# Kernel tuning notes

Measured on AMD Instinct MI355X. Metric: run time of the kernel, lower is better.

## Reference

```python
import jax, jax.numpy as jnp
import numpy as np
from jax import lax

B = 8192          # batched independent VAD frames (original module is batch=1 streaming)
CUTOFF = 129      # STFT_CUTOFF
STRIDE = 128      # STFT_STRIDE
NFFT = 256        # STFT kernel length (inferred: pad 576->640, stride 128 -> 4 frames)
H = 128           # LSTM hidden size


def conv1d(x, w, b=None, stride=1, padding=0):
    # x: [B, Cin, T], w: [Cout, Cin, K]
    y = lax.conv_general_dilated(x, w, (stride,), [(padding, padding)],
                                 dimension_numbers=("NCH", "OIH", "NCH"))
    if b is not None:
        y = y + b[None, :, None]
    return y


def setup_inputs() -> dict:
    key = jax.random.key(0)
    ks = jax.random.split(key, 40)
    f32 = jnp.float32

    def rn(i, shape, scale=0.1):
        return jax.random.normal(ks[i], shape, dtype=f32) * scale

    inp = {
        "audio": jax.random.normal(ks[0], (B, 576), dtype=f32),
        "h": jnp.zeros((B, H), dtype=f32),
        "c": jnp.zeros((B, H), dtype=f32),
        # STFT basis: 129 real + 129 imag cosine/sine rows, kernel 256
        "forward_basis": rn(1, (2 * CUTOFF, 1, NFFT), 0.1),
        # encoder: 4 conv1d+relu blocks (Silero v5 layout)
        "enc_w1": rn(2, (128, 129, 3)), "enc_b1": rn(3, (128,)),
        "enc_w2": rn(4, (64, 128, 3)), "enc_b2": rn(5, (64,)),
        "enc_w3": rn(6, (64, 64, 3)),  "enc_b3": rn(7, (64,)),
        "enc_w4": rn(8, (128, 64, 3)), "enc_b4": rn(9, (128,)),
        # LSTM cell weights
        "wi": rn(10, (H, H)), "wf": rn(11, (H, H)), "wg": rn(12, (H, H)), "wo": rn(13, (H, H)),
        "ui": rn(14, (H, H)), "uf": rn(15, (H, H)), "ug": rn(16, (H, H)), "uo": rn(17, (H, H)),
        "bxi": rn(18, (H,)), "bxf": rn(19, (H,)), "bxg": rn(20, (H,)), "bxo": rn(21, (H,)),
        "bhi": rn(22, (H,)), "bhf": rn(23, (H,)), "bhg": rn(24, (H,)), "bho": rn(25, (H,)),
        # output head: conv1d 128 -> 1, kernel 1
        "conv_w": rn(26, (1, H, 1)), "conv_b": rn(27, (1,)),
    }
    return inp


def reference(audio, h, c, forward_basis,
              enc_w1, enc_b1, enc_w2, enc_b2, enc_w3, enc_b3, enc_w4, enc_b4,
              wi, wf, wg, wo, ui, uf, ug, uo,
              bxi, bxf, bxg, bxo, bhi, bhf, bhg, bho,
              conv_w, conv_b):
    # STFT via strided conv1d on reflect-padded audio
    x = jnp.pad(audio, ((0, 0), (0, 64)), mode="reflect")[:, None, :]   # [B,1,640]
    x = conv1d(x, forward_basis, stride=STRIDE)                          # [B,258,4]
    real, imag = x[:, :CUTOFF, :], x[:, CUTOFF:, :]
    mag = jnp.sqrt(real ** 2 + imag ** 2)                                # [B,129,4]

    # encoder: conv+relu stack, T: 4 -> 4 -> 2 -> 1 -> 1
    e = jax.nn.relu(conv1d(mag, enc_w1, enc_b1, stride=1, padding=1))
    e = jax.nn.relu(conv1d(e, enc_w2, enc_b2, stride=2, padding=1))
    e = jax.nn.relu(conv1d(e, enc_w3, enc_b3, stride=2, padding=1))
    e = jax.nn.relu(conv1d(e, enc_w4, enc_b4, stride=1, padding=1))
    x = e[:, :, 0]                                                       # [B,128]

    lin = lambda v, W, b: v @ W.T + b
    i_gate = jax.nn.sigmoid(lin(x, wi, bxi) + lin(h, ui, bhi))
    f_gate = jax.nn.sigmoid(lin(x, wf, bxf) + lin(h, uf, bhf))
    g_gate = jnp.tanh(lin(x, wg, bxg) + lin(h, ug, bhg))
    o_gate = jax.nn.sigmoid(lin(x, wo, bxo) + lin(h, uo, bho))
    c_out = f_gate * c + i_gate * g_gate
    h_out = o_gate * jnp.tanh(c_out)

    # output head: relu -> conv1d(128->1, k=1) -> sigmoid -> mean over T(=1)
    y = jax.nn.relu(h_out)                                               # [B,128]
    logit = y @ conv_w[0, :, 0] + conv_b[0]                              # [B]
    prob = jax.nn.sigmoid(logit)[:, None]                                # [B,1]
    return prob, h_out, c_out
```

## Files before the change

### kernel.cpp

```cpp
#include <hip/hip_runtime.h>
#include <math.h>

#define BATCH 8192
typedef unsigned short u16;
typedef unsigned int u32;
typedef __attribute__((ext_vector_type(8))) short bf16x8;
typedef __attribute__((ext_vector_type(4))) float f32x4;
typedef __attribute__((ext_vector_type(4))) unsigned short u16x4;

__device__ __forceinline__ float sigm(float v) { return 1.0f / (1.0f + __expf(-v)); }
__device__ __forceinline__ u16 f2bf(float f) {
    union { float f; u32 u; } v; v.f = f;
    u32 r = v.u + 0x7FFFu + ((v.u >> 16) & 1u);
    return (u16)(r >> 16);
}
__device__ __forceinline__ float bf2f(u16 h) {
    union { u32 u; float f; } v; v.u = ((u32)h) << 16; return v.f;
}
__device__ __forceinline__ void split_store4(float4 v, u16* hp, u16* lp) {
    u16 h0 = f2bf(v.x), h1 = f2bf(v.y), h2 = f2bf(v.z), h3 = f2bf(v.w);
    u16x4 hv = {h0, h1, h2, h3};
    u16x4 lv = {f2bf(v.x - bf2f(h0)), f2bf(v.y - bf2f(h1)),
                f2bf(v.z - bf2f(h2)), f2bf(v.w - bf2f(h3))};
    *(u16x4*)hp = hv; *(u16x4*)lp = lv;
}
__device__ __forceinline__ bf16x8 bfrag(const u16* Bf, int nt, int ch, int nch, int lane) {
    return *(const bf16x8*)(Bf + (((size_t)nt * nch + ch) * 64 + lane) * 8);
}
#define MFMA(a, b, c) __builtin_amdgcn_mfma_f32_16x16x32_bf16(a, b, c, 0, 0, 0)

#define S_FBT 69632
#define S_B1  61440
#define S_B2A 16384
#define S_B2B 24576
#define S_B3  8192
#define S_B4  8192
#define S_BL  131072
#define P_FBT 0
#define P_B1  139264
#define P_B2A 262144
#define P_B2B 294912
#define P_B3  344064
#define P_B4  360448
#define P_BL  376832
#define N_PREP 319488

__global__ __launch_bounds__(256) void k_prep(const float* __restrict__ fb,
                                              const float* __restrict__ w1, const float* __restrict__ w2,
                                              const float* __restrict__ w3, const float* __restrict__ w4,
                                              const float* __restrict__ wi, const float* __restrict__ wf,
                                              const float* __restrict__ wg, const float* __restrict__ wo,
                                              const float* __restrict__ ui, const float* __restrict__ uf,
                                              const float* __restrict__ ug, const float* __restrict__ uo,
                                              u16* __restrict__ wsu) {
    const float* Ws[8] = {wi, wf, wg, wo, ui, uf, ug, uo};
    for (int i = blockIdx.x * 256 + threadIdx.x; i < N_PREP; i += gridDim.x * 256) {
        int r = i;
        float v; int P, S, idx;
        if (r < S_FBT) {
            int f = r >> 9, lane = (r & 511) >> 3, e = r & 7;
            int n = (f >> 3) * 16 + (lane & 15), k = (f & 7) * 32 + (lane >> 4) * 8 + e;
            int c = n >> 1, part = n & 1;
            v = (n < 258) ? fb[(size_t)(c + part * 129) * 256 + k] : 0.f;
            P = P_FBT; S = S_FBT; idx = r;
        } else if ((r -= S_FBT) < S_B1) {
            int kk = r / 20480, r2 = r - kk * 20480;
            int f = r2 >> 9, lane = (r2 & 511) >> 3, e = r2 & 7;
            int n = (f / 5) * 16 + (lane & 15), k = (f % 5) * 32 + (lane >> 4) * 8 + e;
            v = (k < 129) ? w1[(size_t)n * 387 + k * 3 + kk] : 0.f;
            P = P_B1; S = S_B1; idx = r;
        } else if ((r -= S_B1) < S_B2A) {
            int f = r >> 9, lane = (r & 511) >> 3, e = r & 7;
            int n = (f >> 3) * 16 + (lane & 15), k = (f & 7) * 32 + (lane >> 4) * 8 + e;
            v = w2[(size_t)n * 384 + (k & 127) * 3 + (k >> 7) + 1];
            P = P_B2A; S = S_B2A; idx = r;
        } else if ((r -= S_B2A) < S_B2B) {
            int f = r >> 9, lane = (r & 511) >> 3, e = r & 7;
            int n = (f / 12) * 16 + (lane & 15), k = (f % 12) * 32 + (lane >> 4) * 8 + e;
            v = w2[(size_t)n * 384 + (k & 127) * 3 + (k >> 7)];
            P = P_B2B; S = S_B2B; idx = r;
        } else if ((r -= S_B2B) < S_B3) {
            int f = r >> 9, lane = (r & 511) >> 3, e = r & 7;
            int n = (f >> 2) * 16 + (lane & 15), k = (f & 3) * 32 + (lane >> 4) * 8 + e;
            v = w3[(size_t)n * 192 + (k & 63) * 3 + (k >> 6) + 1];
            P = P_B3; S = S_B3; idx = r;
        } else if ((r -= S_B3) < S_B4) {
            int f = r >> 9, lane = (r & 511) >> 3, e = r & 7;
            int n = (f >> 1) * 16 + (lane & 15), k = (f & 1) * 32 + (lane >> 4) * 8 + e;
            v = w4[(size_t)n * 192 + k * 3 + 1];
            P = P_B4; S = S_B4; idx = r;
        } else {
            r -= S_B4;
            int f = r >> 9, lane = (r & 511) >> 3, e = r & 7;
            int n = (f >> 3) * 16 + (lane & 15), k = (f & 7) * 32 + (lane >> 4) * 8 + e;
            int g = n >> 7, j = n & 127;
            v = Ws[g + ((k >= 128) ? 4 : 0)][(size_t)j * 128 + (k & 127)];
            P = P_BL; S = S_BL; idx = r;
        }
        u16 h = f2bf(v);
        wsu[P + idx] = h;
        wsu[P + S + idx] = f2bf(v - bf2f(h));
    }
}

__global__ __launch_bounds__(512) void k_all(const float* __restrict__ audio,
                                             const u16* __restrict__ wsu,
                                             const float* __restrict__ hin, const float* __restrict__ cin,
                                             const float* __restrict__ b1, const float* __restrict__ b2,
                                             const float* __restrict__ b3, const float* __restrict__ b4,
                                             const float* __restrict__ bxi, const float* __restrict__ bxf,
                                             const float* __restrict__ bxg, const float* __restrict__ bxo,
                                             const float* __restrict__ bhi, const float* __restrict__ bhf,
                                             const float* __restrict__ bhg, const float* __restrict__ bho,
                                             const float* __restrict__ cw, const float* __restrict__ cb,
                                             float* __restrict__ out) {
    __shared__ __align__(16) u16 uni[32256];
    u16* aAh = uni;
    u16* aAl = uni + 11520;
    u16* mAh = uni;
    u16* mAl = uni + 16128;
    u16* eAh = uni;
    u16* eAl = uni + 8320;
    u16* s2h = uni + 16640;
    u16* s2l = uni + 18816;
    u16* s3h = uni + 20992;
    u16* s3l = uni + 22144;
    u16* xhh = uni + 23296;
    u16* xhl = uni + 27520;
    float* pr = (float*)(uni + 31744);
    const int tid = threadIdx.x;
    const int b0 = blockIdx.x << 4;
    for (int i = tid; i < 16 * 160; i += 512) {
        int bb = i / 160, j4 = (i - bb * 160) * 4;
        const float* ap = audio + (size_t)(b0 + bb) * 576;
        float4 v;
        if (j4 < 576) v = *(const float4*)(ap + j4);
        else { v.x = ap[1150 - j4]; v.y = ap[1149 - j4]; v.z = ap[1148 - j4]; v.w = ap[1147 - j4]; }
        int phys = bb * 720 + j4 + (j4 >> 7) * 8;
        split_store4(v, aAh + phys, aAl + phys);
    }
    __syncthreads();
    const int lane = tid & 63, w = tid >> 6;
    const int m = lane & 15, quad = lane >> 4;
    const u16* fbT = wsu + P_FBT;
    const int tcnt = (w == 7) ? 3 : 2;
    f32x4 acc[4][3];
    #pragma unroll
    for (int mt = 0; mt < 4; ++mt)
        #pragma unroll
        for (int t = 0; t < 3; ++t) acc[mt][t] = (f32x4){0.f, 0.f, 0.f, 0.f};
    for (int ch = 0; ch < 8; ++ch) {
        bf16x8 ah[4], al[4];
        #pragma unroll
        for (int mt = 0; mt < 4; ++mt) {
            int Rm = mt * 16 + m;
            int phys = (Rm >> 2) * 720 + (Rm & 3) * 136 + ch * 32 + quad * 8 + ((ch >= 4) ? 8 : 0);
            ah[mt] = *(const bf16x8*)(aAh + phys);
            al[mt] = *(const bf16x8*)(aAl + phys);
        }
        #pragma unroll
        for (int tt = 0; tt < 3; ++tt) {
            if (tt < tcnt) {
                int t = w * 2 + tt;
                bf16x8 bh = bfrag(fbT, t, ch, 8, lane);
                bf16x8 bl_ = bfrag(fbT + S_FBT, t, ch, 8, lane);
                #pragma unroll
                for (int mt = 0; mt < 4; ++mt) {
                    acc[mt][tt] = MFMA(ah[mt], bh, acc[mt][tt]);
                    acc[mt][tt] = MFMA(ah[mt], bl_, acc[mt][tt]);
                    acc[mt][tt] = MFMA(al[mt], bh, acc[mt][tt]);
                }
            }
        }
    }
    __syncthreads();
    for (int i = tid; i < 16128; i += 512) ((u32*)uni)[i] = 0u;
    __syncthreads();
    #pragma unroll
    for (int tt = 0; tt < 3; ++tt) {
        if (tt < tcnt) {
            int n = (w * 2 + tt) * 16 + m;
            #pragma unroll
            for (int mt = 0; mt < 4; ++mt)
                #pragma unroll
                for (int r = 0; r < 4; ++r) {
                    float vv = acc[mt][tt][r];
                    float s = vv * vv;
                    s += __shfl_xor(s, 1);
                    if (!(n & 1)) {
                        int R = mt * 16 + quad * 4 + r;
                        int bb = R >> 2, t = R & 3, c = n >> 1;
                        float sv = sqrtf(s);
                        u16 h = f2bf(sv);
                        int phys = (bb * 6 + t + 1) * 168 + c;
                        mAh[phys] = h;
                        mAl[phys] = f2bf(sv - bf2f(h));
                    }
                }
        }
    }
    __syncthreads();
    const u16* B1h = wsu + P_B1;
    const u16* B1l = wsu + P_B1 + S_B1;
    f32x4 acc2[4];
    #pragma unroll
    for (int mt = 0; mt < 4; ++mt) acc2[mt] = (f32x4){0.f, 0.f, 0.f, 0.f};
    for (int kk = 0; kk < 3; ++kk) {
        for (int ch = 0; ch < 5; ++ch) {
            bf16x8 bh = bfrag(B1h + kk * 20480, w, ch, 5, lane);
            bf16x8 bl_ = bfrag(B1l + kk * 20480, w, ch, 5, lane);
            #pragma unroll
            for (int mt = 0; mt < 4; ++mt) {
                int Rm = mt * 16 + m;
                int phys = ((Rm >> 2) * 6 + (Rm & 3) + kk) * 168 + ch * 32 + quad * 8;
                bf16x8 ah = *(const bf16x8*)(mAh + phys);
                bf16x8 al = *(const bf16x8*)(mAl + phys);
                acc2[mt] = MFMA(ah, bh, acc2[mt]);
                acc2[mt] = MFMA(ah, bl_, acc2[mt]);
                acc2[mt] = MFMA(al, bh, acc2[mt]);
            }
        }
    }
    __syncthreads();
    {
        int n = w * 16 + m;
        float bv = b1[n];
        #pragma unroll
        for (int mt = 0; mt < 4; ++mt)
            #pragma unroll
            for (int r = 0; r < 4; ++r) {
                int R = mt * 16 + quad * 4 + r;
                float vv = fmaxf(acc2[mt][r] + bv, 0.f);
                u16 h = f2bf(vv);
                int phys = (R >> 2) * 520 + (R & 3) * 128 + n;
                eAh[phys] = h;
                eAl[phys] = f2bf(vv - bf2f(h));
            }
    }
    for (int i = tid; i < 16 * 32; i += 512) {
        int row = i >> 5, c4 = (i & 31) * 4;
        float4 v = *(const float4*)(hin + (size_t)(b0 + row) * 128 + c4);
        split_store4(v, xhh + row * 264 + 128 + c4, xhl + row * 264 + 128 + c4);
    }
    __syncthreads();
    {
        const int isB = w >> 2, nt = w & 3;
        const int awoff = isB ? 128 : 0;
        const int nch = isB ? 12 : 8;
        const u16* Bh = wsu + (isB ? P_B2B : P_B2A);
        const u16* Bl = Bh + (isB ? S_B2B : S_B2A);
        f32x4 a2 = (f32x4){0.f, 0.f, 0.f, 0.f};
        for (int ch = 0; ch < nch; ++ch) {
            int phys = m * 520 + awoff + ch * 32 + quad * 8;
            bf16x8 ah = *(const bf16x8*)(eAh + phys);
            bf16x8 al = *(const bf16x8*)(eAl + phys);
            bf16x8 bh = bfrag(Bh, nt, ch, nch, lane);
            bf16x8 bl_ = bfrag(Bl, nt, ch, nch, lane);
            a2 = MFMA(ah, bh, a2);
            a2 = MFMA(ah, bl_, a2);
            a2 = MFMA(al, bh, a2);
        }
        const int oc = nt * 16 + m;
        const float bv = b2[oc];
        const int col = isB * 64 + oc;
        #pragma unroll
        for (int r = 0; r < 4; ++r) {
            int row = quad * 4 + r;
            float vv = fmaxf(a2[r] + bv, 0.f);
            u16 h = f2bf(vv);
            s2h[row * 136 + col] = h;
            s2l[row * 136 + col] = f2bf(vv - bf2f(h));
        }
    }
    __syncthreads();
    if (w < 4) {
        const u16* Bh = wsu + P_B3;
        const u16* Bl = Bh + S_B3;
        f32x4 a3 = (f32x4){0.f, 0.f, 0.f, 0.f};
        for (int ch = 0; ch < 4; ++ch) {
            int phys = m * 136 + ch * 32 + quad * 8;
            bf16x8 ah = *(const bf16x8*)(s2h + phys);
            bf16x8 al = *(const bf16x8*)(s2l + phys);
            bf16x8 bh = bfrag(Bh, w, ch, 4, lane);
            bf16x8 bl_ = bfrag(Bl, w, ch, 4, lane);
            a3 = MFMA(ah, bh, a3);
            a3 = MFMA(ah, bl_, a3);
            a3 = MFMA(al, bh, a3);
        }
        const int n = w * 16 + m;
        const float bv = b3[n];
        #pragma unroll
        for (int r = 0; r < 4; ++r) {
            int row = quad * 4 + r;
            float vv = fmaxf(a3[r] + bv, 0.f);
            u16 h = f2bf(vv);
            s3h[row * 72 + n] = h;
            s3l[row * 72 + n] = f2bf(vv - bf2f(h));
        }
    }
    __syncthreads();
    {
        const u16* Bh = wsu + P_B4;
        const u16* Bl = Bh + S_B4;
        f32x4 a4 = (f32x4){0.f, 0.f, 0.f, 0.f};
        for (int ch = 0; ch < 2; ++ch) {
            int phys = m * 72 + ch * 32 + quad * 8;
            bf16x8 ah = *(const bf16x8*)(s3h + phys);
            bf16x8 al = *(const bf16x8*)(s3l + phys);
            bf16x8 bh = bfrag(Bh, w, ch, 2, lane);
            bf16x8 bl_ = bfrag(Bl, w, ch, 2, lane);
            a4 = MFMA(ah, bh, a4);
            a4 = MFMA(ah, bl_, a4);
            a4 = MFMA(al, bh, a4);
        }
        const int n = w * 16 + m;
        const float bv = b4[n];
        #pragma unroll
        for (int r = 0; r < 4; ++r) {
            int row = quad * 4 + r;
            float vv = fmaxf(a4[r] + bv, 0.f);
            u16 h = f2bf(vv);
            xhh[row * 264 + n] = h;
            xhl[row * 264 + n] = f2bf(vv - bf2f(h));
        }
    }
    __syncthreads();
    {
        const u16* BLh = wsu + P_BL;
        const u16* BLl = BLh + S_BL;
        f32x4 ag[4];
        #pragma unroll
        for (int g = 0; g < 4; ++g) ag[g] = (f32x4){0.f, 0.f, 0.f, 0.f};
        #pragma unroll 2
        for (int ch = 0; ch < 8; ++ch) {
            int phys = m * 264 + ch * 32 + quad * 8;
            bf16x8 ah = *(const bf16x8*)(xhh + phys);
            bf16x8 al = *(const bf16x8*)(xhl + phys);
            #pragma unroll
            for (int g = 0; g < 4; ++g) {
                int nt = g * 8 + w;
                bf16x8 bh = bfrag(BLh, nt, ch, 8, lane);
                bf16x8 bl_ = bfrag(BLl, nt, ch, 8, lane);
                ag[g] = MFMA(ah, bh, ag[g]);
                ag[g] = MFMA(ah, bl_, ag[g]);
                ag[g] = MFMA(al, bh, ag[g]);
            }
        }
        float partial[4];
        const int j = w * 16 + m;
        const float bi = bxi[j] + bhi[j];
        const float bff = bxf[j] + bhf[j];
        const float bgg = bxg[j] + bhg[j];
        const float boo = bxo[j] + bho[j];
        const float cwj = cw[j];
        #pragma unroll
        for (int r = 0; r < 4; ++r) {
            const int b = b0 + quad * 4 + r;
            const float ig = sigm(ag[0][r] + bi);
            const float fg = sigm(ag[1][r] + bff);
            const float gg = tanhf(ag[2][r] + bgg);
            const float og = sigm(ag[3][r] + boo);
            const float ci = cin[(size_t)b * 128 + j];
            const float co = fg * ci + ig * gg;
            const float ho = og * tanhf(co);
            out[(size_t)BATCH + (size_t)b * 128 + j] = ho;
            out[(size_t)BATCH + (size_t)BATCH * 128 + (size_t)b * 128 + j] = co;
            partial[r] = fmaxf(ho, 0.f) * cwj;
        }
        #pragma unroll
        for (int off = 1; off < 16; off <<= 1)
            #pragma unroll
            for (int r = 0; r < 4; ++r) partial[r] += __shfl_xor(partial[r], off);
        if (m == 0) {
            #pragma unroll
            for (int r = 0; r < 4; ++r) pr[w * 16 + quad * 4 + r] = partial[r];
        }
    }
    __syncthreads();
    if (tid < 16) {
        float s = cb[0];
        #pragma unroll
        for (int g = 0; g < 8; ++g) s += pr[g * 16 + tid];
        out[b0 + tid] = sigm(s);
    }
}

extern "C" void kernel_launch(void* const* d_in, const int* in_sizes, int n_in,
                              void* d_out, int out_size, void* d_ws, size_t ws_size,
                              hipStream_t stream) {
    const float* audio = (const float*)d_in[0];
    const float* hin   = (const float*)d_in[1];
    const float* cin   = (const float*)d_in[2];
    const float* fb    = (const float*)d_in[3];
    const float* w1    = (const float*)d_in[4];
    const float* b1    = (const float*)d_in[5];
    const float* w2    = (const float*)d_in[6];
    const float* b2    = (const float*)d_in[7];
    const float* w3    = (const float*)d_in[8];
    const float* b3    = (const float*)d_in[9];
    const float* w4    = (const float*)d_in[10];
    const float* b4    = (const float*)d_in[11];
    const float* wi    = (const float*)d_in[12];
    const float* wf    = (const float*)d_in[13];
    const float* wg    = (const float*)d_in[14];
    const float* wo    = (const float*)d_in[15];
    const float* ui    = (const float*)d_in[16];
    const float* uf    = (const float*)d_in[17];
    const float* ug    = (const float*)d_in[18];
    const float* uo    = (const float*)d_in[19];
    const float* bxi   = (const float*)d_in[20];
    const float* bxf   = (const float*)d_in[21];
    const float* bxg   = (const float*)d_in[22];
    const float* bxo   = (const float*)d_in[23];
    const float* bhi   = (const float*)d_in[24];
    const float* bhf   = (const float*)d_in[25];
    const float* bhg   = (const float*)d_in[26];
    const float* bho   = (const float*)d_in[27];
    const float* cw    = (const float*)d_in[28];
    const float* cb    = (const float*)d_in[29];
    float* out = (float*)d_out;

    u16* wsu = (u16*)d_ws;

    k_prep<<<640, 256, 0, stream>>>(fb, w1, w2, w3, w4, wi, wf, wg, wo, ui, uf, ug, uo, wsu);
    k_all<<<BATCH / 16, 512, 0, stream>>>(audio, wsu, hin, cin, b1, b2, b3, b4,
                                          bxi, bxf, bxg, bxo, bhi, bhf, bhg, bho,
                                          cw, cb, out);
}
```

Measured before the change: 176.7 us.

## Re-tile MFMA work across waves for fragment reuse and add occupancy hint

Warps now split the STFT and encoder-1 GEMMs 2D (row-half by column-group), so each wave loads fewer A fragments and reuses them across more N tiles. The later encoder and LSTM stages run on half the waves, each handling two N tiles, so every A fragment load feeds twice as many MFMAs. Launch bounds now request 4 blocks per SM to push register allocation down. In exchange, idle waves reduce parallelism in the tail stages, and the larger per-wave accumulator arrays may spill under the tighter register cap.

```diff
diff --git a/kernel.cpp b/kernel.cpp
--- a/kernel.cpp
+++ b/kernel.cpp
@@ -103,7 +103,7 @@
     }
 }
 
-__global__ __launch_bounds__(512) void k_all(const float* __restrict__ audio,
+__global__ __launch_bounds__(512, 4) void k_all(const float* __restrict__ audio,
                                              const u16* __restrict__ wsu,
                                              const float* __restrict__ hin, const float* __restrict__ cin,
                                              const float* __restrict__ b1, const float* __restrict__ b2,
@@ -142,33 +142,35 @@
     __syncthreads();
     const int lane = tid & 63, w = tid >> 6;
     const int m = lane & 15, quad = lane >> 4;
+    const int wh = w >> 2;
+    const int g  = w & 3;
     const u16* fbT = wsu + P_FBT;
-    const int tcnt = (w == 7) ? 3 : 2;
-    f32x4 acc[4][3];
+    const int tcnt = (g == 3) ? 5 : 4;
+    f32x4 acc[2][5];
     #pragma unroll
-    for (int mt = 0; mt < 4; ++mt)
-        #pragma unroll
-        for (int t = 0; t < 3; ++t) acc[mt][t] = (f32x4){0.f, 0.f, 0.f, 0.f};
+    for (int mt2 = 0; mt2 < 2; ++mt2)
+        #pragma unroll
+        for (int t = 0; t < 5; ++t) acc[mt2][t] = (f32x4){0.f, 0.f, 0.f, 0.f};
     for (int ch = 0; ch < 8; ++ch) {
-        bf16x8 ah[4], al[4];
-        #pragma unroll
-        for (int mt = 0; mt < 4; ++mt) {
-            int Rm = mt * 16 + m;
+        bf16x8 ah[2], al[2];
+        #pragma unroll
+        for (int mt2 = 0; mt2 < 2; ++mt2) {
+            int Rm = (wh * 2 + mt2) * 16 + m;
             int phys = (Rm >> 2) * 720 + (Rm & 3) * 136 + ch * 32 + quad * 8 + ((ch >= 4) ? 8 : 0);
-            ah[mt] = *(const bf16x8*)(aAh + phys);
-            al[mt] = *(const bf16x8*)(aAl + phys);
-        }
-        #pragma unroll
-        for (int tt = 0; tt < 3; ++tt) {
+            ah[mt2] = *(const bf16x8*)(aAh + phys);
+            al[mt2] = *(const bf16x8*)(aAl + phys);
+        }
+        #pragma unroll
+        for (int tt = 0; tt < 5; ++tt) {
             if (tt < tcnt) {
-                int t = w * 2 + tt;
+                int t = g * 4 + tt;
                 bf16x8 bh = bfrag(fbT, t, ch, 8, lane);
                 bf16x8 bl_ = bfrag(fbT + S_FBT, t, ch, 8, lane);
                 #pragma unroll
-                for (int mt = 0; mt < 4; ++mt) {
-                    acc[mt][tt] = MFMA(ah[mt], bh, acc[mt][tt]);
-                    acc[mt][tt] = MFMA(ah[mt], bl_, acc[mt][tt]);
-                    acc[mt][tt] = MFMA(al[mt], bh, acc[mt][tt]);
+                for (int mt2 = 0; mt2 < 2; ++mt2) {
+                    acc[mt2][tt] = MFMA(ah[mt2], bh, acc[mt2][tt]);
+                    acc[mt2][tt] = MFMA(ah[mt2], bl_, acc[mt2][tt]);
+                    acc[mt2][tt] = MFMA(al[mt2], bh, acc[mt2][tt]);
                 }
             }
         }
@@ -177,18 +179,18 @@
     for (int i = tid; i < 16128; i += 512) ((u32*)uni)[i] = 0u;
     __syncthreads();
     #pragma unroll
-    for (int tt = 0; tt < 3; ++tt) {
+    for (int tt = 0; tt < 5; ++tt) {
         if (tt < tcnt) {
-            int n = (w * 2 + tt) * 16 + m;
-            #pragma unroll
-            for (int mt = 0; mt < 4; ++mt)
+            int n = (g * 4 + tt) * 16 + m;
+            #pragma unroll
+            for (int mt2 = 0; mt2 < 2; ++mt2)
                 #pragma unroll
                 for (int r = 0; r < 4; ++r) {
-                    float vv = acc[mt][tt][r];
+                    float vv = acc[mt2][tt][r];
                     float s = vv * vv;
                     s += __shfl_xor(s, 1);
                     if (!(n & 1)) {
-                        int R = mt * 16 + quad * 4 + r;
+                        int R = (wh * 2 + mt2) * 16 + quad * 4 + r;
                         int bb = R >> 2, t = R & 3, c = n >> 1;
                         float sv = sqrtf(s);
                         u16 h = f2bf(sv);
@@ -202,35 +204,46 @@
     __syncthreads();
     const u16* B1h = wsu + P_B1;
     const u16* B1l = wsu + P_B1 + S_B1;
-    f32x4 acc2[4];
+    f32x4 acc2[2][2];
     #pragma unroll
-    for (int mt = 0; mt < 4; ++mt) acc2[mt] = (f32x4){0.f, 0.f, 0.f, 0.f};
+    for (int mt2 = 0; mt2 < 2; ++mt2)
+        #pragma unroll
+        for (int d = 0; d < 2; ++d) acc2[mt2][d] = (f32x4){0.f, 0.f, 0.f, 0.f};
     for (int kk = 0; kk < 3; ++kk) {
         for (int ch = 0; ch < 5; ++ch) {
-            bf16x8 bh = bfrag(B1h + kk * 20480, w, ch, 5, lane);
-            bf16x8 bl_ = bfrag(B1l + kk * 20480, w, ch, 5, lane);
-            #pragma unroll
-            for (int mt = 0; mt < 4; ++mt) {
-                int Rm = mt * 16 + m;
+            bf16x8 ah[2], al[2];
+            #pragma unroll
+            for (int mt2 = 0; mt2 < 2; ++mt2) {
+                int Rm = (wh * 2 + mt2) * 16 + m;
                 int phys = ((Rm >> 2) * 6 + (Rm & 3) + kk) * 168 + ch * 32 + quad * 8;
-                bf16x8 ah = *(const bf16x8*)(mAh + phys);
-                bf16x8 al = *(const bf16x8*)(mAl + phys);
-                acc2[mt] = MFMA(ah, bh, acc2[mt]);
-                acc2[mt] = MFMA(ah, bl_, acc2[mt]);
-                acc2[mt] = MFMA(al, bh, acc2[mt]);
-            }
-        }
-    }
-    __syncthreads();
-    {
-        int n = w * 16 + m;
+                ah[mt2] = *(const bf16x8*)(mAh + phys);
+                al[mt2] = *(const bf16x8*)(mAl + phys);
+            }
+            #pragma unroll
+            for (int d = 0; d < 2; ++d) {
+                int nt = 2 * g + d;
+                bf16x8 bh = bfrag(B1h + kk * 20480, nt, ch, 5, lane);
+                bf16x8 bl_ = bfrag(B1l + kk * 20480, nt, ch, 5, lane);
+                #pragma unroll
+                for (int mt2 = 0; mt2 < 2; ++mt2) {
+                    acc2[mt2][d] = MFMA(ah[mt2], bh, acc2[mt2][d]);
+                    acc2[mt2][d] = MFMA(ah[mt2], bl_, acc2[mt2][d]);
+                    acc2[mt2][d] = MFMA(al[mt2], bh, acc2[mt2][d]);
+                }
+            }
+        }
+    }
+    __syncthreads();
+    #pragma unroll
+    for (int d = 0; d < 2; ++d) {
+        int n = (2 * g + d) * 16 + m;
         float bv = b1[n];
         #pragma unroll
-        for (int mt = 0; mt < 4; ++mt)
+        for (int mt2 = 0; mt2 < 2; ++mt2)
             #pragma unroll
             for (int r = 0; r < 4; ++r) {
-                int R = mt * 16 + quad * 4 + r;
-                float vv = fmaxf(acc2[mt][r] + bv, 0.f);
+                int R = (wh * 2 + mt2) * 16 + quad * 4 + r;
+                float vv = fmaxf(acc2[mt2][d][r] + bv, 0.f);
                 u16 h = f2bf(vv);
                 int phys = (R >> 2) * 520 + (R & 3) * 128 + n;
                 eAh[phys] = h;
@@ -243,129 +256,162 @@
         split_store4(v, xhh + row * 264 + 128 + c4, xhl + row * 264 + 128 + c4);
     }
     __syncthreads();
-    {
-        const int isB = w >> 2, nt = w & 3;
+    if (w < 4) {
+        const int isB = w >> 1, ntp = w & 1;
         const int awoff = isB ? 128 : 0;
         const int nch = isB ? 12 : 8;
         const u16* Bh = wsu + (isB ? P_B2B : P_B2A);
         const u16* Bl = Bh + (isB ? S_B2B : S_B2A);
-        f32x4 a2 = (f32x4){0.f, 0.f, 0.f, 0.f};
+        f32x4 a2[2];
+        a2[0] = (f32x4){0.f, 0.f, 0.f, 0.f};
+        a2[1] = (f32x4){0.f, 0.f, 0.f, 0.f};
         for (int ch = 0; ch < nch; ++ch) {
             int phys = m * 520 + awoff + ch * 32 + quad * 8;
             bf16x8 ah = *(const bf16x8*)(eAh + phys);
             bf16x8 al = *(const bf16x8*)(eAl + phys);
-            bf16x8 bh = bfrag(Bh, nt, ch, nch, lane);
-            bf16x8 bl_ = bfrag(Bl, nt, ch, nch, lane);
-            a2 = MFMA(ah, bh, a2);
-            a2 = MFMA(ah, bl_, a2);
-            a2 = MFMA(al, bh, a2);
-        }
-        const int oc = nt * 16 + m;
-        const float bv = b2[oc];
-        const int col = isB * 64 + oc;
-        #pragma unroll
-        for (int r = 0; r < 4; ++r) {
-            int row = quad * 4 + r;
-            float vv = fmaxf(a2[r] + bv, 0.f);
-            u16 h = f2bf(vv);
-            s2h[row * 136 + col] = h;
-            s2l[row * 136 + col] = f2bf(vv - bf2f(h));
-        }
-    }
-    __syncthreads();
-    if (w < 4) {
+            #pragma unroll
+            for (int d = 0; d < 2; ++d) {
+                int nt = 2 * ntp + d;
+                bf16x8 bh = bfrag(Bh, nt, ch, nch, lane);
+                bf16x8 bl_ = bfrag(Bl, nt, ch, nch, lane);
+                a2[d] = MFMA(ah, bh, a2[d]);
+                a2[d] = MFMA(ah, bl_, a2[d]);
+                a2[d] = MFMA(al, bh, a2[d]);
+            }
+        }
+        #pragma unroll
+        for (int d = 0; d < 2; ++d) {
+            const int oc = (2 * ntp + d) * 16 + m;
+            const float bv = b2[oc];
+            const int col = isB * 64 + oc;
+            #pragma unroll
+            for (int r = 0; r < 4; ++r) {
+                int row = quad * 4 + r;
+                float vv = fmaxf(a2[d][r] + bv, 0.f);
+                u16 h = f2bf(vv);
+                s2h[row * 136 + col] = h;
+                s2l[row * 136 + col] = f2bf(vv - bf2f(h));
+            }
+        }
+    }
+    __syncthreads();
+    if (w < 2) {
         const u16* Bh = wsu + P_B3;
         const u16* Bl = Bh + S_B3;
-        f32x4 a3 = (f32x4){0.f, 0.f, 0.f, 0.f};
+        f32x4 a3[2];
+        a3[0] = (f32x4){0.f, 0.f, 0.f, 0.f};
+        a3[1] = (f32x4){0.f, 0.f, 0.f, 0.f};
         for (int ch = 0; ch < 4; ++ch) {
             int phys = m * 136 + ch * 32 + quad * 8;
             bf16x8 ah = *(const bf16x8*)(s2h + phys);
             bf16x8 al = *(const bf16x8*)(s2l + phys);
-            bf16x8 bh = bfrag(Bh, w, ch, 4, lane);
-            bf16x8 bl_ = bfrag(Bl, w, ch, 4, lane);
-            a3 = MFMA(ah, bh, a3);
-            a3 = MFMA(ah, bl_, a3);
-            a3 = MFMA(al, bh, a3);
-        }
-        const int n = w * 16 + m;
-        const float bv = b3[n];
-        #pragma unroll
-        for (int r = 0; r < 4; ++r) {
-            int row = quad * 4 + r;
-            float vv = fmaxf(a3[r] + bv, 0.f);
-            u16 h = f2bf(vv);
-            s3h[row * 72 + n] = h;
-            s3l[row * 72 + n] = f2bf(vv - bf2f(h));
-        }
-    }
-    __syncthreads();
-    {
+            #pragma unroll
+            for (int d = 0; d < 2; ++d) {
+                int nt = 2 * w + d;
+                bf16x8 bh = bfrag(Bh, nt, ch, 4, lane);
+                bf16x8 bl_ = bfrag(Bl, nt, ch, 4, lane);
+                a3[d] = MFMA(ah, bh, a3[d]);
+                a3[d] = MFMA(ah, bl_, a3[d]);
+                a3[d] = MFMA(al, bh, a3[d]);
+            }
+        }
+        #pragma unroll
+        for (int d = 0; d < 2; ++d) {
+            const int n = (2 * w + d) * 16 + m;
+            const float bv = b3[n];
+            #pragma unroll
+            for (int r = 0; r < 4; ++r) {
+                int row = quad * 4 + r;
+                float vv = fmaxf(a3[d][r] + bv, 0.f);
+                u16 h = f2bf(vv);
+                s3h[row * 72 + n] = h;
+                s3l[row * 72 + n] = f2bf(vv - bf2f(h));
+            }
+        }
+    }
+    __syncthreads();
+    if (w < 4) {
         const u16* Bh = wsu + P_B4;
         const u16* Bl = Bh + S_B4;
-        f32x4 a4 = (f32x4){0.f, 0.f, 0.f, 0.f};
+        f32x4 a4[2];
+        a4[0] = (f32x4){0.f, 0.f, 0.f, 0.f};
+        a4[1] = (f32x4){0.f, 0.f, 0.f, 0.f};
         for (int ch = 0; ch < 2; ++ch) {
             int phys = m * 72 + ch * 32 + quad * 8;
             bf16x8 ah = *(const bf16x8*)(s3h + phys);
             bf16x8 al = *(const bf16x8*)(s3l + phys);
-            bf16x8 bh = bfrag(Bh, w, ch, 2, lane);
-            bf16x8 bl_ = bfrag(Bl, w, ch, 2, lane);
-            a4 = MFMA(ah, bh, a4);
-            a4 = MFMA(ah, bl_, a4);
-            a4 = MFMA(al, bh, a4);
-        }
-        const int n = w * 16 + m;
-        const float bv = b4[n];
-        #pragma unroll
-        for (int r = 0; r < 4; ++r) {
-            int row = quad * 4 + r;
-            float vv = fmaxf(a4[r] + bv, 0.f);
-            u16 h = f2bf(vv);
-            xhh[row * 264 + n] = h;
-            xhl[row * 264 + n] = f2bf(vv - bf2f(h));
-        }
-    }
-    __syncthreads();
-    {
+            #pragma unroll
+            for (int d = 0; d < 2; ++d) {
+                int nt = 2 * w + d;
+                bf16x8 bh = bfrag(Bh, nt, ch, 2, lane);
+                bf16x8 bl_ = bfrag(Bl, nt, ch, 2, lane);
+                a4[d] = MFMA(ah, bh, a4[d]);
+                a4[d] = MFMA(ah, bl_, a4[d]);
+                a4[d] = MFMA(al, bh, a4[d]);
+            }
+        }
+        #pragma unroll
+        for (int d = 0; d < 2; ++d) {
+            const int n = (2 * w + d) * 16 + m;
+            const float bv = b4[n];
+            #pragma unroll
+            for (int r = 0; r < 4; ++r) {
+                int row = quad * 4 + r;
+                float vv = fmaxf(a4[d][r] + bv, 0.f);
+                u16 h = f2bf(vv);
+                xhh[row * 264 + n] = h;
+                xhl[row * 264 + n] = f2bf(vv - bf2f(h));
+            }
+        }
+    }
+    __syncthreads();
+    if (w < 4) {
         const u16* BLh = wsu + P_BL;
         const u16* BLl = BLh + S_BL;
-        f32x4 ag[4];
-        #pragma unroll
-        for (int g = 0; g < 4; ++g) ag[g] = (f32x4){0.f, 0.f, 0.f, 0.f};
-        #pragma unroll 2
+        f32x4 ag[4][2];
+        #pragma unroll
+        for (int gg = 0; gg < 4; ++gg)
+            #pragma unroll
+            for (int d = 0; d < 2; ++d) ag[gg][d] = (f32x4){0.f, 0.f, 0.f, 0.f};
         for (int ch = 0; ch < 8; ++ch) {
             int phys = m * 264 + ch * 32 + quad * 8;
             bf16x8 ah = *(const bf16x8*)(xhh + phys);
             bf16x8 al = *(const bf16x8*)(xhl + phys);
             #pragma unroll
-            for (int g = 0; g < 4; ++g) {
-                int nt = g * 8 + w;
-                bf16x8 bh = bfrag(BLh, nt, ch, 8, lane);
-                bf16x8 bl_ = bfrag(BLl, nt, ch, 8, lane);
-                ag[g] = MFMA(ah, bh, ag[g]);
-                ag[g] = MFMA(ah, bl_, ag[g]);
-                ag[g] = MFMA(al, bh, ag[g]);
-            }
-        }
-        float partial[4];
-        const int j = w * 16 + m;
-        const float bi = bxi[j] + bhi[j];
-        const float bff = bxf[j] + bhf[j];
-        const float bgg = bxg[j] + bhg[j];
-        const float boo = bxo[j] + bho[j];
-        const float cwj = cw[j];
-        #pragma unroll
-        for (int r = 0; r < 4; ++r) {
-            const int b = b0 + quad * 4 + r;
-            const float ig = sigm(ag[0][r] + bi);
-            const float fg = sigm(ag[1][r] + bff);
-            const float gg = tanhf(ag[2][r] + bgg);
-            const float og = sigm(ag[3][r] + boo);
-            const float ci = cin[(size_t)b * 128 + j];
-            const float co = fg * ci + ig * gg;
-            const float ho = og * tanhf(co);
-            out[(size_t)BATCH + (size_t)b * 128 + j] = ho;
-            out[(size_t)BATCH + (size_t)BATCH * 128 + (size_t)b * 128 + j] = co;
-            partial[r] = fmaxf(ho, 0.f) * cwj;
+            for (int gg = 0; gg < 4; ++gg)
+                #pragma unroll
+                for (int d = 0; d < 2; ++d) {
+                    int nt = gg * 8 + 2 * w + d;
+                    bf16x8 bh = bfrag(BLh, nt, ch, 8, lane);
+                    bf16x8 bl_ = bfrag(BLl, nt, ch, 8, lane);
+                    ag[gg][d] = MFMA(ah, bh, ag[gg][d]);
+                    ag[gg][d] = MFMA(ah, bl_, ag[gg][d]);
+                    ag[gg][d] = MFMA(al, bh, ag[gg][d]);
+                }
+        }
+        float partial[4] = {0.f, 0.f, 0.f, 0.f};
+        #pragma unroll
+        for (int d = 0; d < 2; ++d) {
+            const int j = (2 * w + d) * 16 + m;
+            const float bi = bxi[j] + bhi[j];
+            const float bff = bxf[j] + bhf[j];
+            const float bgg = bxg[j] + bhg[j];
+            const float boo = bxo[j] + bho[j];
+            const float cwj = cw[j];
+            #pragma unroll
+            for (int r = 0; r < 4; ++r) {
+                const int b = b0 + quad * 4 + r;
+                const float ig = sigm(ag[0][d][r] + bi);
+                const float fg = sigm(ag[1][d][r] + bff);
+                const float gg = tanhf(ag[2][d][r] + bgg);
+                const float og = sigm(ag[3][d][r] + boo);
+                const float ci = cin[(size_t)b * 128 + j];
+                const float co = fg * ci + ig * gg;
+                const float ho = og * tanhf(co);
+                out[(size_t)BATCH + (size_t)b * 128 + j] = ho;
+                out[(size_t)BATCH + (size_t)BATCH * 128 + (size_t)b * 128 + j] = co;
+                partial[r] += fmaxf(ho, 0.f) * cwj;
+            }
         }
         #pragma unroll
         for (int off = 1; off < 16; off <<= 1)
@@ -380,7 +426,7 @@
     if (tid < 16) {
         float s = cb[0];
         #pragma unroll
-        for (int g = 0; g < 8; ++g) s += pr[g * 16 + tid];
+        for (int gg = 0; gg < 4; ++gg) s += pr[gg * 16 + tid];
         out[b0 + tid] = sigm(s);
     }
 }
```

Measured after the change: 186.8 us. 1.06x slower.
